# Optimization experiments

Hardware: AMD Instinct MI355X
Metric: run time of the kernel (lower is better)

The kernel has to match this reference:

```python
import jax, jax.numpy as jnp
import numpy as np

B, T, R, A = 4, 40, 2000, 36864
H = W = 64
C = 256
PP = 7
RED = 16.0
NCLS = 21
NPOS = 64   # rois_per_image*B//4
NNEG = 192  # rois_per_image*B*3//4
DH = 1024

def _iou(b1, b2):
    # boxes are (top,left,bottom,right)
    t = jnp.maximum(b1[..., 0], b2[..., 0])
    l = jnp.maximum(b1[..., 1], b2[..., 1])
    b = jnp.minimum(b1[..., 2], b2[..., 2])
    r = jnp.minimum(b1[..., 3], b2[..., 3])
    inter = jnp.clip(b - t, 0.0) * jnp.clip(r - l, 0.0)
    a1 = (b1[..., 2] - b1[..., 0]) * (b1[..., 3] - b1[..., 1])
    a2 = (b2[..., 2] - b2[..., 0]) * (b2[..., 3] - b2[..., 1])
    return inter / (a1 + a2 - inter)

def _smooth_l1(p, t):
    d = jnp.abs(p - t)
    return jnp.mean(jnp.where(d < 1.0, 0.5 * d * d, d - 0.5))

def _roi_pool(fm, rois):
    # fm [B,C,H,W], rois [N,5] = (img_id, top,left,bottom,right) in feature-map coords
    fmt = jnp.transpose(fm, (0, 2, 3, 1))  # [B,H,W,C]
    n = rois[:, 0].astype(jnp.int32)[:, None, None]
    t, l, b, r = rois[:, 1], rois[:, 2], rois[:, 3], rois[:, 4]
    g = (jnp.arange(PP, dtype=fm.dtype) + 0.5) / PP
    ys = jnp.clip(t[:, None] + g * (b - t)[:, None], 0.0, H - 1.0)
    xs = jnp.clip(l[:, None] + g * (r - l)[:, None], 0.0, W - 1.0)
    y0 = jnp.floor(ys).astype(jnp.int32)
    x0 = jnp.floor(xs).astype(jnp.int32)
    y1 = jnp.minimum(y0 + 1, H - 1)
    x1 = jnp.minimum(x0 + 1, W - 1)
    wy = (ys - y0)[:, :, None, None]
    wx = (xs - x0)[:, None, :, None]
    def gat(yi, xi):
        return fmt[n, yi[:, :, None], xi[:, None, :], :]  # [N,PP,PP,C]
    v = (gat(y0, x0) * (1 - wy) * (1 - wx) + gat(y0, x1) * (1 - wy) * wx
         + gat(y1, x0) * wy * (1 - wx) + gat(y1, x1) * wy * wx)
    return v.reshape(v.shape[0], -1)  # [N, PP*PP*C]

def _forward(nms_reg, nms_cls, feature_maps, bboxes, classes, anchors, rpn_reg, rpn_cls, W1, b1, Wr, br, Wc, bc):
    # ---------------- RPN trainer: anchor/target matching ----------------
    iou_a = _iou(bboxes[:, :, None, :], anchors[None, None, :, :])   # [B,T,A]
    max_iou = jnp.max(iou_a, axis=1)                                  # [B,A]
    tidx = jnp.argmax(iou_a, axis=1)
    max_tgt = jnp.take_along_axis(bboxes, jnp.broadcast_to(tidx[:, :, None], (B, A, 4)), axis=1)
    mask = (max_iou > 0.5).reshape(-1)
    pos = jnp.nonzero(mask, size=128)[0]        # first 128 positives, flat order (matches cls[mask][:128])
    neg = jnp.nonzero(~mask, size=256 - B)[0]   # torch quirk: 256 - len(mask_matched) = 256 - B
    clsf = rpn_cls.reshape(-1)
    logits = jnp.concatenate([clsf[pos], clsf[neg]])
    lbl = jnp.concatenate([jnp.ones(128, dtype=logits.dtype), jnp.zeros(256 - B, dtype=logits.dtype)])
    rpn_cls_loss = jnp.mean(jnp.maximum(logits, 0) - logits * lbl + jnp.log1p(jnp.exp(-jnp.abs(logits))))
    anc_f = jnp.broadcast_to(anchors[None], (B, A, 4)).reshape(-1, 4)
    rpn_reg_loss = _smooth_l1(rpn_reg.reshape(-1, 4)[pos], max_tgt.reshape(-1, 4)[pos] - anc_f[pos]) / 4.0

    # ------------- RCNN trainer: proposal matching + sampling -------------
    iou_r = _iou(nms_reg[:, None, :, :], bboxes[:, :, None, :])  # [B,T,R]
    iou_m = jnp.max(iou_r, axis=1)                               # [B,R]
    ridx = jnp.argmax(iou_r, axis=1)
    iou_f = iou_m.reshape(-1)
    posr = jnp.nonzero(iou_f > 0.5, size=NPOS)[0]                # first NPOS positives, flat order
    negscore = jnp.where(iou_f <= 0.5, iou_f, -jnp.inf)
    negr = jax.lax.top_k(negscore, NNEG)[1]                      # negatives sorted by IoU descending
    cls_g = jnp.take_along_axis(classes, ridx, axis=1).reshape(-1)
    cls_s = jnp.concatenate([cls_g[posr], jnp.zeros(NNEG, dtype=cls_g.dtype)])
    imid = jnp.repeat(jnp.arange(B, dtype=nms_reg.dtype), R)
    nmsf = nms_reg.reshape(-1, 4)
    sel = jnp.concatenate([posr, negr])
    rois = jnp.concatenate([imid[sel][:, None], nmsf[sel]], axis=1)  # [256,5]
    feat = _roi_pool(feature_maps, rois)
    hmid = jax.nn.relu(feat @ W1 + b1)
    rreg = hmid @ Wr + br
    rcls = hmid @ Wc + bc
    logp = jax.nn.log_softmax(rcls, axis=-1)
    rcnn_cls_loss = -jnp.mean(jnp.take_along_axis(logp, cls_s[:, None], axis=1))
    posb = nmsf[posr]
    rounded = jnp.concatenate([jnp.floor(posb[:, :2] * RED), jnp.ceil(posb[:, 2:] * RED)], axis=1) / RED
    mb = jnp.take_along_axis(bboxes, jnp.broadcast_to(ridx[:, :, None], (B, R, 4)), axis=1).reshape(-1, 4)[posr]
    tgt = mb - rounded
    pr = rreg[:NPOS]
    rcnn_reg_loss = sum(_smooth_l1(pr[:, c], tgt[:, c]) for c in range(4)) / 4.0
    offset = sum(jnp.mean(jnp.abs(pr[:, c] - tgt[:, c])) for c in range(4)) / 4.0
    acc = jnp.mean((jnp.argmax(rcls[:NPOS], axis=-1) == cls_s[:NPOS]).astype(jnp.float32))
    return rpn_cls_loss, rpn_reg_loss, rcnn_cls_loss, rcnn_reg_loss, acc, offset

def _boxes(k, shape):
    k1, k2 = jax.random.split(k)
    c = jax.random.uniform(k1, shape + (2,), minval=10.0, maxval=54.0)
    h = jax.random.uniform(k2, shape + (2,), minval=3.0, maxval=8.0)
    return jnp.concatenate([c - h, c + h], axis=-1)  # (top,left,bottom,right)

def setup_inputs():
    key = jax.random.key(0)
    ks = jax.random.split(key, 13)
    base = _boxes(ks[0], (T,))
    shift = jax.random.uniform(ks[1], (B, T, 2), minval=-0.2, maxval=0.2)
    bboxes = base[None] + jnp.concatenate([shift, shift], axis=-1)  # guarantees >=128 RPN positives
    classes = jax.random.randint(ks[2], (B, T), 1, NCLS)
    anchors = _boxes(ks[3], (A,)).at[:T].set(base)
    nms_reg = _boxes(ks[4], (B, R))
    shift2 = jax.random.uniform(ks[5], (B, T, 2), minval=-0.1, maxval=0.1)
    nms_reg = nms_reg.at[:, :T].set(bboxes + jnp.concatenate([shift2, shift2], axis=-1))  # >=64 RCNN positives
    nms_cls = jax.random.normal(ks[6], (B, R))
    feature_maps = jax.random.normal(ks[7], (B, C, H, W))
    rpn_reg = 0.1 * jax.random.normal(ks[8], (B, A, 4))
    rpn_cls = jax.random.normal(ks[9], (B, A))
    D = PP * PP * C
    W1 = jax.random.normal(ks[10], (D, DH)) * float(1.0 / np.sqrt(D))
    b1 = jnp.zeros((DH,))
    Wr = jax.random.normal(ks[11], (DH, 4)) * float(1.0 / np.sqrt(DH))
    br = jnp.zeros((4,))
    Wc = jax.random.normal(ks[12], (DH, NCLS)) * float(1.0 / np.sqrt(DH))
    bc = jnp.zeros((NCLS,))
    return dict(nms_reg=nms_reg, nms_cls=nms_cls, feature_maps=feature_maps, bboxes=bboxes,
                classes=classes, anchors=anchors, rpn_reg=rpn_reg, rpn_cls=rpn_cls,
                W1=W1, b1=b1, Wr=Wr, br=br, Wc=Wc, bc=bc)

def reference(nms_reg, nms_cls, feature_maps, bboxes, classes, anchors, rpn_reg, rpn_cls, W1, b1, Wr, br, Wc, bc):
    return _forward(nms_reg, nms_cls, feature_maps, bboxes, classes, anchors, rpn_reg, rpn_cls, W1, b1, Wr, br, Wc, bc)
```

## Files before the change

kernel.cpp:

```cpp
#include <hip/hip_runtime.h>

typedef unsigned short u16;
typedef unsigned long long u64;

constexpr int cB = 4, cT = 40, cR = 2000, cA = 36864;
constexpr int cH = 64, cW = 64, cC = 256, cPP = 7;
constexpr int cNCLS = 21, cNPOS = 64, cNNEG = 192, cDH = 1024;
constexpr int cD = cPP * cPP * cC;
constexpr int cBA = cB * cA;
constexpr int cBR = cB * cR;
constexpr int NW64 = cBA / 64;
constexpr int SPLITS = 8;
constexpr int KCH = cD / SPLITS;
constexpr unsigned POSKEY = 0x007FFFFFu;

constexpr size_t O_TIDX  = 0;
constexpr size_t O_MASKW = (size_t)cBA * 4;
constexpr size_t O_FMT   = 0;
constexpr size_t O_CPART = 0;
constexpr size_t O_PERS  = 8388608;
constexpr size_t O_SEL   = O_PERS;
constexpr size_t O_CLS   = O_PERS + 1024;
constexpr size_t O_ROIS  = O_PERS + 2048;
constexpr size_t O_TGT   = O_PERS + 6144;
constexpr size_t O_FEAT  = O_PERS + 8192;
constexpr size_t O_HMID  = O_FEAT + (size_t)256 * cD * 2;
constexpr size_t O_RREG  = O_HMID + (size_t)256 * cDH * 4;
constexpr size_t O_RCLS  = O_RREG + 4096;
constexpr size_t O_KEYS  = O_RCLS + 24576;
constexpr size_t O_RIDXG = O_KEYS + 32000;

__device__ __forceinline__ float b2f(u16 u) {
  return __uint_as_float(((unsigned)u) << 16);
}
__device__ __forceinline__ u16 f2b(float f) {
  unsigned x = __float_as_uint(f);
  unsigned r = x + 0x7FFFu + ((x >> 16) & 1u);
  return (u16)(r >> 16);
}
__device__ __forceinline__ unsigned f2key(float f) {
  unsigned b = __float_as_uint(f);
  return b ^ ((b & 0x80000000u) ? 0xFFFFFFFFu : 0x80000000u);
}

typedef __attribute__((ext_vector_type(8))) short short8;
typedef __attribute__((ext_vector_type(4))) float f32x4;

__global__ void k_rpn_iou(const float* __restrict__ bboxes, const float* __restrict__ anchors,
                          int* __restrict__ tidx, u64* __restrict__ maskw) {
  __shared__ float sb[cT * 4];
  int b = blockIdx.x / 144;
  if (threadIdx.x < cT * 4) sb[threadIdx.x] = bboxes[b * cT * 4 + threadIdx.x];
  __syncthreads();
  int i = blockIdx.x * 256 + threadIdx.x;
  int a = i - b * cA;
  float4 av = ((const float4*)anchors)[a];
  float at = av.x, al = av.y, ab = av.z, ar = av.w;
  float area_a = (ab - at) * (ar - al);
  float best = -1.0f; int bi = 0;
  for (int t = 0; t < cT; ++t) {
    float bt = sb[t * 4], bl = sb[t * 4 + 1], bbv = sb[t * 4 + 2], brv = sb[t * 4 + 3];
    float ih = fmaxf(fminf(bbv, ab) - fmaxf(bt, at), 0.0f);
    float iw = fmaxf(fminf(brv, ar) - fmaxf(bl, al), 0.0f);
    float inter = ih * iw;
    float a1 = (bbv - bt) * (brv - bl);
    float iou = inter / (a1 + area_a - inter);
    if (iou > best) { best = iou; bi = t; }
  }
  tidx[i] = bi;
  u64 bal = __ballot(best > 0.5f);
  if ((threadIdx.x & 63) == 0) maskw[i >> 6] = bal;
}

__global__ __launch_bounds__(1024) void k_rpn_sample_loss(
    const u64* __restrict__ maskw, const int* __restrict__ tidx,
    const float* __restrict__ rpn_cls, const float* __restrict__ rpn_reg,
    const float* __restrict__ bboxes, const float* __restrict__ anchors,
    float* __restrict__ out) {
  __shared__ u64 s_w[NW64];
  __shared__ int s_pre[144];
  __shared__ int s_cw[144];
  __shared__ int s_pos[128];
  __shared__ int s_neg[252];
  __shared__ float s_cls, s_reg;
  int tid = threadIdx.x, lane = tid & 63, w = tid >> 6;
  for (int k = tid; k < NW64; k += 1024) s_w[k] = maskw[k];
  if (tid < 128) s_pos[tid] = 0;
  if (tid < 252) s_neg[tid] = 0;
  if (tid == 0) { s_cls = 0.0f; s_reg = 0.0f; }
  __syncthreads();
  if (tid < 144) {
    int c = 0;
    #pragma unroll
    for (int k2 = 0; k2 < 16; ++k2) c += __popcll(s_w[tid * 16 + k2]);
    s_cw[tid] = c;
  }
  __syncthreads();
  if (tid == 0) {
    int run = 0;
    for (int ch = 0; ch < 144; ++ch) { s_pre[ch] = run; run += s_cw[ch]; }
  }
  __syncthreads();
  u64 lmask = (1ULL << lane) - 1ULL;
  for (int ch = w; ch < 144; ch += 16) {
    int pbase = s_pre[ch];
    int nbase = ch * 1024 - pbase;
    if (pbase >= 128 && nbase >= 252) continue;
    int pc = 0;
    #pragma unroll
    for (int s2 = 0; s2 < 16; ++s2) {
      u64 word = s_w[ch * 16 + s2];
      bool m = (word >> lane) & 1ULL;
      int prefP = __popcll(word & lmask);
      int idx = ch * 1024 + s2 * 64 + lane;
      if (m) {
        int g = pbase + pc + prefP;
        if (g < 128) s_pos[g] = idx;
      } else {
        int g = nbase + (s2 * 64 + lane) - (pc + prefP);
        if (g < 252) s_neg[g] = idx;
      }
      pc += __popcll(word);
    }
  }
  __syncthreads();
  if (tid < 380) {
    int flat; float lbl;
    if (tid < 128) { flat = s_pos[tid]; lbl = 1.0f; }
    else           { flat = s_neg[tid - 128]; lbl = 0.0f; }
    float l = rpn_cls[flat];
    float term = fmaxf(l, 0.0f) - l * lbl + log1pf(expf(-fabsf(l)));
    atomicAdd(&s_cls, term);
  }
  if (tid < 512) {
    int j = tid >> 2, c = tid & 3;
    int flat = s_pos[j];
    int b = flat / cA, a = flat - b * cA;
    int t = tidx[flat];
    float p = rpn_reg[flat * 4 + c];
    float tg = bboxes[(b * cT + t) * 4 + c] - anchors[a * 4 + c];
    float d = fabsf(p - tg);
    float sl = (d < 1.0f) ? 0.5f * d * d : d - 0.5f;
    atomicAdd(&s_reg, sl);
  }
  __syncthreads();
  if (tid == 0) {
    out[0] = s_cls / 380.0f;
    out[1] = s_reg / 512.0f / 4.0f;
  }
}

__global__ void k_rcnn_iou(const float* __restrict__ nms_reg, const float* __restrict__ bboxes,
                           unsigned* __restrict__ keys, int* __restrict__ ridx) {
  __shared__ float sb[cB * cT * 4];
  for (int j = threadIdx.x; j < cB * cT * 4; j += 256) sb[j] = bboxes[j];
  __syncthreads();
  int i = blockIdx.x * 256 + threadIdx.x;
  if (i >= cBR) return;
  int b = i / cR;
  float4 nv = ((const float4*)nms_reg)[i];
  float nt = nv.x, nl = nv.y, nb = nv.z, nr = nv.w;
  float area_n = (nb - nt) * (nr - nl);
  float best = -1.0f; int bi = 0;
  for (int t = 0; t < cT; ++t) {
    const float* bx = &sb[(b * cT + t) * 4];
    float ih = fmaxf(fminf(bx[2], nb) - fmaxf(bx[0], nt), 0.0f);
    float iw = fmaxf(fminf(bx[3], nr) - fmaxf(bx[1], nl), 0.0f);
    float inter = ih * iw;
    float a1 = (bx[2] - bx[0]) * (bx[3] - bx[1]);
    float iou = inter / (a1 + area_n - inter);
    if (iou > best) { best = iou; bi = t; }
  }
  keys[i] = (best <= 0.5f) ? f2key(best) : POSKEY;
  ridx[i] = bi;
}

__global__ __launch_bounds__(1024) void k_rcnn_select(
    const unsigned* __restrict__ keysg, const int* __restrict__ ridxg,
    const float* __restrict__ nms_reg, const float* __restrict__ bboxes,
    const int* __restrict__ classes,
    int* __restrict__ sel, int* __restrict__ cls_s,
    float* __restrict__ rois, float* __restrict__ tgt) {
  __shared__ unsigned s_key[cBR];
  __shared__ int s_hist[4096];
  __shared__ int s_pc[128];
  __shared__ int s_wsum[16], s_wsuf[16];
  __shared__ int s_posr[64], s_negr[cNNEG];
  __shared__ int s_bStar, s_over, s_cnt;
  int tid = threadIdx.x, lane = tid & 63, w = tid >> 6;
  u64 lmask = (1ULL << lane) - 1ULL;

  for (int i = tid; i < cBR; i += 1024) s_key[i] = keysg[i];
  if (tid < 64) s_posr[tid] = 0;
  __syncthreads();

  {
    int myv = 0; int mypre[8];
    #pragma unroll
    for (int p = 0; p < 8; ++p) {
      int i = p * 1024 + tid;
      bool v = (i < cBR) && (s_key[i] == POSKEY);
      u64 bal = __ballot(v);
      if (lane == 0) s_pc[p * 16 + w] = __popcll(bal);
      mypre[p] = __popcll(bal & lmask);
      myv |= v ? (1 << p) : 0;
    }
    __syncthreads();
    if (tid == 0) {
      int run = 0;
      for (int k = 0; k < 128; ++k) { int t = s_pc[k]; s_pc[k] = run; run += t; }
    }
    __syncthreads();
    #pragma unroll
    for (int p = 0; p < 8; ++p) {
      if (myv & (1 << p)) {
        int g = s_pc[p * 16 + w] + mypre[p];
        if (g < 64) s_posr[g] = p * 1024 + tid;
      }
    }
  }

  unsigned thr = 0; int G = 0;
  int need = cNNEG;
  #pragma unroll
  for (int lvl = 0; lvl < 3; ++lvl) {
    __syncthreads();
    #pragma unroll
    for (int k = 0; k < 4; ++k) s_hist[tid * 4 + k] = 0;
    __syncthreads();
    #pragma unroll
    for (int p = 0; p < 8; ++p) {
      int i = p * 1024 + tid;
      if (i < cBR) {
        unsigned key = s_key[i];
        int bkt = -1;
        if (lvl == 0) bkt = key >> 20;
        else if (lvl == 1) { if ((key >> 20) == (thr >> 20)) bkt = (key >> 8) & 0xFFF; }
        else { if ((key >> 8) == (thr >> 8)) bkt = (key & 0xFF) << 4; }
        if (bkt >= 0) atomicAdd(&s_hist[bkt], 1);
      }
    }
    __syncthreads();
    int local0 = s_hist[tid * 4 + 0], local1 = s_hist[tid * 4 + 1];
    int local2 = s_hist[tid * 4 + 2], local3 = s_hist[tid * 4 + 3];
    int lsum = local0 + local1 + local2 + local3;
    int x = lsum;
    #pragma unroll
    for (int off = 1; off < 64; off <<= 1) {
      int t = __shfl_down(x, off, 64);
      if (lane + off < 64) x += t;
    }
    if (lane == 0) s_wsum[w] = x;
    __syncthreads();
    if (tid == 0) {
      int run = 0;
      for (int wi = 15; wi >= 0; --wi) { s_wsuf[wi] = run; run += s_wsum[wi]; }
    }
    __syncthreads();
    int above = s_wsuf[w] + (x - lsum);
    int run = above;
    int loc[4] = {local3, local2, local1, local0};
    #pragma unroll
    for (int j = 0; j < 4; ++j) {
      int S = run + loc[j];
      if (run < need && S >= need) { s_bStar = tid * 4 + (3 - j); s_over = run; }
      run = S;
    }
    __syncthreads();
    int bS = s_bStar, ov = s_over;
    if (lvl == 0) thr = ((unsigned)bS) << 20;
    else if (lvl == 1) thr |= ((unsigned)bS) << 8;
    else thr |= ((unsigned)bS) >> 4;
    G += ov;
    need -= ov;
  }

  if (tid == 0) s_cnt = 0;
  __syncthreads();
  #pragma unroll
  for (int p = 0; p < 8; ++p) {
    int i = p * 1024 + tid;
    if (i < cBR && s_key[i] > thr) {
      int slot = atomicAdd(&s_cnt, 1);
      s_negr[slot] = i;
    }
  }
  {
    __syncthreads();
    int myv = 0; int mypre[8];
    #pragma unroll
    for (int p = 0; p < 8; ++p) {
      int i = p * 1024 + tid;
      bool v = (i < cBR) && (s_key[i] == thr);
      u64 bal = __ballot(v);
      if (lane == 0) s_pc[p * 16 + w] = __popcll(bal);
      mypre[p] = __popcll(bal & lmask);
      myv |= v ? (1 << p) : 0;
    }
    __syncthreads();
    if (tid == 0) {
      int run = 0;
      for (int k = 0; k < 128; ++k) { int t = s_pc[k]; s_pc[k] = run; run += t; }
    }
    __syncthreads();
    #pragma unroll
    for (int p = 0; p < 8; ++p) {
      if (myv & (1 << p)) {
        int g = s_pc[p * 16 + w] + mypre[p];
        if (g < need) s_negr[G + g] = p * 1024 + tid;
      }
    }
  }
  __syncthreads();

  if (tid < 256) {
    int flat = (tid < 64) ? s_posr[tid] : s_negr[tid - 64];
    sel[tid] = flat;
    int b = flat / cR;
    #pragma unroll
    for (int c = 0; c < 4; ++c) rois[tid * 4 + c] = nms_reg[flat * 4 + c];
    cls_s[tid] = (tid < 64) ? classes[b * cT + ridxg[flat]] : 0;
    if (tid < 64) {
      int mt = ridxg[flat];
      #pragma unroll
      for (int c = 0; c < 4; ++c) {
        float v = nms_reg[flat * 4 + c];
        float rr = ((c < 2) ? floorf(v * 16.0f) : ceilf(v * 16.0f)) / 16.0f;
        float mbv = bboxes[(b * cT + mt) * 4 + c];
        tgt[tid * 4 + c] = mbv - rr;
      }
    }
  }
}

__global__ void k_fmt(const float* __restrict__ fm, u16* __restrict__ fmt) {
  __shared__ float tile[32][33];
  int b = blockIdx.z;
  int p0 = blockIdx.x * 32, c0 = blockIdx.y * 32;
  int tx = threadIdx.x, ty = threadIdx.y;
  tile[ty][tx] = fm[((size_t)b * cC + (c0 + ty)) * (cH * cW) + p0 + tx];
  __syncthreads();
  fmt[((size_t)b * (cH * cW) + (p0 + ty)) * cC + c0 + tx] = f2b(tile[tx][ty]);
}

__global__ void k_roi_pool(const u16* __restrict__ fmt, const float* __restrict__ rois,
                           const int* __restrict__ sel, u16* __restrict__ feat) {
  int j = blockIdx.x;
  int py = blockIdx.y;
  int c = threadIdx.x;
  int flat = sel[j];
  int n = flat / cR;
  float t = rois[j * 4 + 0], l = rois[j * 4 + 1];
  float bb = rois[j * 4 + 2], r = rois[j * 4 + 3];
  const u16* base = fmt + (size_t)n * (cH * cW) * cC;
  float gy = (py + 0.5f) / (float)cPP;
  float ys = fminf(fmaxf(t + gy * (bb - t), 0.0f), 63.0f);
  int y0 = (int)floorf(ys);
  int y1 = min(y0 + 1, 63);
  float wy = ys - (float)y0;
  #pragma unroll
  for (int px = 0; px < cPP; ++px) {
    float gx = (px + 0.5f) / (float)cPP;
    float xs = fminf(fmaxf(l + gx * (r - l), 0.0f), 63.0f);
    int x0 = (int)floorf(xs);
    int x1 = min(x0 + 1, 63);
    float wx = xs - (float)x0;
    float f00 = b2f(base[(y0 * cW + x0) * cC + c]);
    float f01 = b2f(base[(y0 * cW + x1) * cC + c]);
    float f10 = b2f(base[(y1 * cW + x0) * cC + c]);
    float f11 = b2f(base[(y1 * cW + x1) * cC + c]);
    float v = f00 * (1.0f - wy) * (1.0f - wx) + f01 * (1.0f - wy) * wx +
              f10 * wy * (1.0f - wx) + f11 * wy * wx;
    feat[((size_t)j * 49 + py * cPP + px) * cC + c] = f2b(v);
  }
}

__global__ __launch_bounds__(256) void k_gemm1(const u16* __restrict__ feat, const float* __restrict__ W1,
                                               float* __restrict__ Cpart) {
  __shared__ u16 As[128][56];
  __shared__ u16 Bs[64][56];
  int tid = threadIdx.x;
  int n0 = blockIdx.x * 64;
  int kb0 = blockIdx.y * KCH;
  int m0 = blockIdx.z * 128;
  int lane = tid & 63, w = tid >> 6;
  int r = lane & 15, q = lane >> 4;
  f32x4 acc[2][4] = {};
  int arow = tid >> 1, ak = (tid & 1) * 16;
  int bk = tid >> 3, bn = (tid & 7) * 8;
  uint4 ra0, ra1;
  float4 rb0, rb1;
  {
    const u16* ap = &feat[(size_t)(m0 + arow) * cD + kb0 + ak];
    ra0 = *(const uint4*)ap; ra1 = *(const uint4*)(ap + 8);
    const float* bp = &W1[(size_t)(kb0 + bk) * cDH + n0 + bn];
    rb0 = *(const float4*)bp; rb1 = *(const float4*)(bp + 4);
  }
  for (int kc = 0; kc < KCH / 32; ++kc) {
    __syncthreads();
    *(uint4*)&As[arow][ak] = ra0;
    *(uint4*)&As[arow][ak + 8] = ra1;
    Bs[bn + 0][bk] = f2b(rb0.x); Bs[bn + 1][bk] = f2b(rb0.y);
    Bs[bn + 2][bk] = f2b(rb0.z); Bs[bn + 3][bk] = f2b(rb0.w);
    Bs[bn + 4][bk] = f2b(rb1.x); Bs[bn + 5][bk] = f2b(rb1.y);
    Bs[bn + 6][bk] = f2b(rb1.z); Bs[bn + 7][bk] = f2b(rb1.w);
    if (kc + 1 < KCH / 32) {
      int kb = kb0 + (kc + 1) * 32;
      const u16* ap = &feat[(size_t)(m0 + arow) * cD + kb + ak];
      ra0 = *(const uint4*)ap; ra1 = *(const uint4*)(ap + 8);
      const float* bp = &W1[(size_t)(kb + bk) * cDH + n0 + bn];
      rb0 = *(const float4*)bp; rb1 = *(const float4*)(bp + 4);
    }
    __syncthreads();
    short8 a[2], bfr[4];
    #pragma unroll
    for (int mt = 0; mt < 2; ++mt) a[mt] = *(const short8*)&As[w * 32 + mt * 16 + r][q * 8];
    #pragma unroll
    for (int nt = 0; nt < 4; ++nt) bfr[nt] = *(const short8*)&Bs[nt * 16 + r][q * 8];
    #pragma unroll
    for (int mt = 0; mt < 2; ++mt)
      #pragma unroll
      for (int nt = 0; nt < 4; ++nt)
        acc[mt][nt] = __builtin_amdgcn_mfma_f32_16x16x32_bf16(a[mt], bfr[nt], acc[mt][nt], 0, 0, 0);
  }
  float* Cp = Cpart + (size_t)blockIdx.y * 256 * cDH;
  #pragma unroll
  for (int mt = 0; mt < 2; ++mt) {
    #pragma unroll
    for (int nt = 0; nt < 4; ++nt) {
      #pragma unroll
      for (int rg = 0; rg < 4; ++rg) {
        int row = m0 + w * 32 + mt * 16 + q * 4 + rg;
        int col = n0 + nt * 16 + r;
        Cp[(size_t)row * cDH + col] = acc[mt][nt][rg];
      }
    }
  }
}

__global__ void k_bias_relu(const float* __restrict__ Cpart, const float* __restrict__ b1,
                            float* __restrict__ hmid) {
  int i = blockIdx.x * 256 + threadIdx.x;
  float v = b1[i & (cDH - 1)];
  #pragma unroll
  for (int s = 0; s < SPLITS; ++s) v += Cpart[(size_t)s * 256 * cDH + i];
  hmid[i] = fmaxf(v, 0.0f);
}

__global__ void k_gemm2(const float* __restrict__ hmid, const float* __restrict__ Wr, const float* __restrict__ br,
                        const float* __restrict__ Wc, const float* __restrict__ bc,
                        float* __restrict__ rreg, float* __restrict__ rcls) {
  int w = threadIdx.x >> 6, lane = threadIdx.x & 63;
  int row = blockIdx.x * 4 + w;
  float part[25];
  #pragma unroll
  for (int c = 0; c < 25; ++c) part[c] = 0.0f;
  for (int k = lane; k < cDH; k += 64) {
    float h = hmid[(size_t)row * cDH + k];
    #pragma unroll
    for (int c = 0; c < 4; ++c) part[c] += h * Wr[k * 4 + c];
    #pragma unroll
    for (int c = 0; c < 21; ++c) part[4 + c] += h * Wc[k * 21 + c];
  }
  #pragma unroll
  for (int off = 32; off; off >>= 1) {
    #pragma unroll
    for (int c = 0; c < 25; ++c) part[c] += __shfl_down(part[c], off, 64);
  }
  if (lane == 0) {
    #pragma unroll
    for (int c = 0; c < 4; ++c) rreg[row * 4 + c] = part[c] + br[c];
    #pragma unroll
    for (int c = 0; c < 21; ++c) rcls[row * 21 + c] = part[4 + c] + bc[c];
  }
}

__global__ void k_final(const float* __restrict__ rcls, const float* __restrict__ rreg,
                        const int* __restrict__ cls_s, const float* __restrict__ tgt,
                        float* __restrict__ out) {
  __shared__ float s_cls, s_acc, s_sl1, s_off;
  int tid = threadIdx.x;
  if (tid == 0) { s_cls = 0.0f; s_acc = 0.0f; s_sl1 = 0.0f; s_off = 0.0f; }
  __syncthreads();
  {
    int row = tid;
    float m = -INFINITY;
    for (int c = 0; c < cNCLS; ++c) m = fmaxf(m, rcls[row * cNCLS + c]);
    float sum = 0.0f;
    for (int c = 0; c < cNCLS; ++c) sum += expf(rcls[row * cNCLS + c] - m);
    float lse = m + logf(sum);
    float closs = lse - rcls[row * cNCLS + cls_s[row]];
    atomicAdd(&s_cls, closs);
  }
  if (tid < 64) {
    int am = 0; float bv = rcls[tid * cNCLS];
    for (int c = 1; c < cNCLS; ++c) {
      float v = rcls[tid * cNCLS + c];
      if (v > bv) { bv = v; am = c; }
    }
    if (am == cls_s[tid]) atomicAdd(&s_acc, 1.0f);
    float sl = 0.0f, of = 0.0f;
    #pragma unroll
    for (int c = 0; c < 4; ++c) {
      float d = fabsf(rreg[tid * 4 + c] - tgt[tid * 4 + c]);
      sl += (d < 1.0f) ? 0.5f * d * d : d - 0.5f;
      of += d;
    }
    atomicAdd(&s_sl1, sl);
    atomicAdd(&s_off, of);
  }
  __syncthreads();
  if (tid == 0) {
    out[2] = s_cls / 256.0f;
    out[3] = s_sl1 / 256.0f;
    out[4] = s_acc / 64.0f;
    out[5] = s_off / 256.0f;
  }
}

extern "C" void kernel_launch(void* const* d_in, const int* in_sizes, int n_in,
                              void* d_out, int out_size, void* d_ws, size_t ws_size,
                              hipStream_t stream) {
  const float* nms_reg = (const float*)d_in[0];
  const float* fm      = (const float*)d_in[2];
  const float* bboxes  = (const float*)d_in[3];
  const int*   classes = (const int*)d_in[4];
  const float* anchors = (const float*)d_in[5];
  const float* rpn_reg = (const float*)d_in[6];
  const float* rpn_cls = (const float*)d_in[7];
  const float* W1      = (const float*)d_in[8];
  const float* b1      = (const float*)d_in[9];
  const float* Wr      = (const float*)d_in[10];
  const float* br      = (const float*)d_in[11];
  const float* Wc      = (const float*)d_in[12];
  const float* bc      = (const float*)d_in[13];
  float* out = (float*)d_out;
  char* ws = (char*)d_ws;

  int*      tidx  = (int*)(ws + O_TIDX);
  u64*      maskw = (u64*)(ws + O_MASKW);
  u16*      fmt   = (u16*)(ws + O_FMT);
  float*    Cpart = (float*)(ws + O_CPART);
  int*      sel   = (int*)(ws + O_SEL);
  int*      clss  = (int*)(ws + O_CLS);
  float*    rois  = (float*)(ws + O_ROIS);
  float*    tgt   = (float*)(ws + O_TGT);
  u16*      feat  = (u16*)(ws + O_FEAT);
  float*    hmid  = (float*)(ws + O_HMID);
  float*    rreg  = (float*)(ws + O_RREG);
  float*    rcls  = (float*)(ws + O_RCLS);
  unsigned* keys  = (unsigned*)(ws + O_KEYS);
  int*      ridxg = (int*)(ws + O_RIDXG);

  k_rpn_iou<<<cBA / 256, 256, 0, stream>>>(bboxes, anchors, tidx, maskw);
  k_rpn_sample_loss<<<1, 1024, 0, stream>>>(maskw, tidx, rpn_cls, rpn_reg, bboxes, anchors, out);

  k_rcnn_iou<<<(cBR + 255) / 256, 256, 0, stream>>>(nms_reg, bboxes, keys, ridxg);
  k_rcnn_select<<<1, 1024, 0, stream>>>(keys, ridxg, nms_reg, bboxes, classes, sel, clss, rois, tgt);

  k_fmt<<<dim3(cH * cW / 32, cC / 32, cB), dim3(32, 32), 0, stream>>>(fm, fmt);
  k_roi_pool<<<dim3(256, cPP), 256, 0, stream>>>(fmt, rois, sel, feat);
  k_gemm1<<<dim3(16, SPLITS, 2), 256, 0, stream>>>(feat, W1, Cpart);
  k_bias_relu<<<(256 * cDH) / 256, 256, 0, stream>>>(Cpart, b1, hmid);
  k_gemm2<<<64, 256, 0, stream>>>(hmid, Wr, br, Wc, bc, rreg, rcls);
  k_final<<<1, 256, 0, stream>>>(rcls, rreg, clss, tgt, out);
}
```

Measured before the change: 226.4 us.

## Merge IoU and select kernels, retile transpose and GEMM1, fuse bias-ReLU into heads

Combines the RPN and RCNN IoU kernels into one launch and the two single-block selection kernels into a single two-block launch, so the two sequential selection passes run concurrently. The feature-map transpose now uses 64x64 tiles and writes packed 16-byte bf16 stores. GEMM1 drops to 64-row M tiles with twice as many blocks and an XOR-swizzled B tile in shared memory to reduce bank conflicts. The split-K reduction, bias and ReLU are folded into the head GEMV, which removes the hmid buffer and one launch at the cost of re-reading the split partials inside the heads kernel.

```diff
diff --git a/kernel.cpp b/kernel.cpp
--- a/kernel.cpp
+++ b/kernel.cpp
@@ -24,8 +24,7 @@
 constexpr size_t O_ROIS  = O_PERS + 2048;
 constexpr size_t O_TGT   = O_PERS + 6144;
 constexpr size_t O_FEAT  = O_PERS + 8192;
-constexpr size_t O_HMID  = O_FEAT + (size_t)256 * cD * 2;
-constexpr size_t O_RREG  = O_HMID + (size_t)256 * cDH * 4;
+constexpr size_t O_RREG  = O_FEAT + (size_t)256 * cD * 2;
 constexpr size_t O_RCLS  = O_RREG + 4096;
 constexpr size_t O_KEYS  = O_RCLS + 24576;
 constexpr size_t O_RIDXG = O_KEYS + 32000;
@@ -46,301 +45,318 @@
 typedef __attribute__((ext_vector_type(8))) short short8;
 typedef __attribute__((ext_vector_type(4))) float f32x4;
 
-__global__ void k_rpn_iou(const float* __restrict__ bboxes, const float* __restrict__ anchors,
-                          int* __restrict__ tidx, u64* __restrict__ maskw) {
-  __shared__ float sb[cT * 4];
-  int b = blockIdx.x / 144;
-  if (threadIdx.x < cT * 4) sb[threadIdx.x] = bboxes[b * cT * 4 + threadIdx.x];
-  __syncthreads();
-  int i = blockIdx.x * 256 + threadIdx.x;
-  int a = i - b * cA;
-  float4 av = ((const float4*)anchors)[a];
-  float at = av.x, al = av.y, ab = av.z, ar = av.w;
-  float area_a = (ab - at) * (ar - al);
-  float best = -1.0f; int bi = 0;
-  for (int t = 0; t < cT; ++t) {
-    float bt = sb[t * 4], bl = sb[t * 4 + 1], bbv = sb[t * 4 + 2], brv = sb[t * 4 + 3];
-    float ih = fmaxf(fminf(bbv, ab) - fmaxf(bt, at), 0.0f);
-    float iw = fmaxf(fminf(brv, ar) - fmaxf(bl, al), 0.0f);
-    float inter = ih * iw;
-    float a1 = (bbv - bt) * (brv - bl);
-    float iou = inter / (a1 + area_a - inter);
-    if (iou > best) { best = iou; bi = t; }
-  }
-  tidx[i] = bi;
-  u64 bal = __ballot(best > 0.5f);
-  if ((threadIdx.x & 63) == 0) maskw[i >> 6] = bal;
-}
-
-__global__ __launch_bounds__(1024) void k_rpn_sample_loss(
+__global__ void k_ious(const float* __restrict__ bboxes, const float* __restrict__ anchors,
+                       const float* __restrict__ nms_reg,
+                       int* __restrict__ tidx, u64* __restrict__ maskw,
+                       unsigned* __restrict__ keys, int* __restrict__ ridxg) {
+  __shared__ float sb[cB * cT * 4];
+  if (blockIdx.x < 576) {
+    int b = blockIdx.x / 144;
+    if (threadIdx.x < cT * 4) sb[threadIdx.x] = bboxes[b * cT * 4 + threadIdx.x];
+    __syncthreads();
+    int i = blockIdx.x * 256 + threadIdx.x;
+    int a = i - b * cA;
+    float4 av = ((const float4*)anchors)[a];
+    float at = av.x, al = av.y, ab = av.z, ar = av.w;
+    float area_a = (ab - at) * (ar - al);
+    float best = -1.0f; int bi = 0;
+    for (int t = 0; t < cT; ++t) {
+      float bt = sb[t * 4], bl = sb[t * 4 + 1], bbv = sb[t * 4 + 2], brv = sb[t * 4 + 3];
+      float ih = fmaxf(fminf(bbv, ab) - fmaxf(bt, at), 0.0f);
+      float iw = fmaxf(fminf(brv, ar) - fmaxf(bl, al), 0.0f);
+      float inter = ih * iw;
+      float a1 = (bbv - bt) * (brv - bl);
+      float iou = inter / (a1 + area_a - inter);
+      if (iou > best) { best = iou; bi = t; }
+    }
+    tidx[i] = bi;
+    u64 bal = __ballot(best > 0.5f);
+    if ((threadIdx.x & 63) == 0) maskw[i >> 6] = bal;
+  } else {
+    for (int j = threadIdx.x; j < cB * cT * 4; j += 256) sb[j] = bboxes[j];
+    __syncthreads();
+    int i = (blockIdx.x - 576) * 256 + threadIdx.x;
+    if (i >= cBR) return;
+    int b = i / cR;
+    float4 nv = ((const float4*)nms_reg)[i];
+    float nt = nv.x, nl = nv.y, nb = nv.z, nr = nv.w;
+    float area_n = (nb - nt) * (nr - nl);
+    float best = -1.0f; int bi = 0;
+    for (int t = 0; t < cT; ++t) {
+      const float* bx = &sb[(b * cT + t) * 4];
+      float ih = fmaxf(fminf(bx[2], nb) - fmaxf(bx[0], nt), 0.0f);
+      float iw = fmaxf(fminf(bx[3], nr) - fmaxf(bx[1], nl), 0.0f);
+      float inter = ih * iw;
+      float a1 = (bx[2] - bx[0]) * (bx[3] - bx[1]);
+      float iou = inter / (a1 + area_n - inter);
+      if (iou > best) { best = iou; bi = t; }
+    }
+    keys[i] = (best <= 0.5f) ? f2key(best) : POSKEY;
+    ridxg[i] = bi;
+  }
+}
+
+__global__ __launch_bounds__(1024) void k_select(
     const u64* __restrict__ maskw, const int* __restrict__ tidx,
     const float* __restrict__ rpn_cls, const float* __restrict__ rpn_reg,
     const float* __restrict__ bboxes, const float* __restrict__ anchors,
+    const unsigned* __restrict__ keysg, const int* __restrict__ ridxg,
+    const float* __restrict__ nms_reg, const int* __restrict__ classes,
+    int* __restrict__ sel, int* __restrict__ cls_s,
+    float* __restrict__ rois, float* __restrict__ tgt,
     float* __restrict__ out) {
-  __shared__ u64 s_w[NW64];
-  __shared__ int s_pre[144];
-  __shared__ int s_cw[144];
-  __shared__ int s_pos[128];
-  __shared__ int s_neg[252];
-  __shared__ float s_cls, s_reg;
-  int tid = threadIdx.x, lane = tid & 63, w = tid >> 6;
-  for (int k = tid; k < NW64; k += 1024) s_w[k] = maskw[k];
-  if (tid < 128) s_pos[tid] = 0;
-  if (tid < 252) s_neg[tid] = 0;
-  if (tid == 0) { s_cls = 0.0f; s_reg = 0.0f; }
-  __syncthreads();
-  if (tid < 144) {
-    int c = 0;
-    #pragma unroll
-    for (int k2 = 0; k2 < 16; ++k2) c += __popcll(s_w[tid * 16 + k2]);
-    s_cw[tid] = c;
-  }
-  __syncthreads();
-  if (tid == 0) {
-    int run = 0;
-    for (int ch = 0; ch < 144; ++ch) { s_pre[ch] = run; run += s_cw[ch]; }
-  }
-  __syncthreads();
-  u64 lmask = (1ULL << lane) - 1ULL;
-  for (int ch = w; ch < 144; ch += 16) {
-    int pbase = s_pre[ch];
-    int nbase = ch * 1024 - pbase;
-    if (pbase >= 128 && nbase >= 252) continue;
-    int pc = 0;
-    #pragma unroll
-    for (int s2 = 0; s2 < 16; ++s2) {
-      u64 word = s_w[ch * 16 + s2];
-      bool m = (word >> lane) & 1ULL;
-      int prefP = __popcll(word & lmask);
-      int idx = ch * 1024 + s2 * 64 + lane;
-      if (m) {
-        int g = pbase + pc + prefP;
-        if (g < 128) s_pos[g] = idx;
-      } else {
-        int g = nbase + (s2 * 64 + lane) - (pc + prefP);
-        if (g < 252) s_neg[g] = idx;
-      }
-      pc += __popcll(word);
-    }
-  }
-  __syncthreads();
-  if (tid < 380) {
-    int flat; float lbl;
-    if (tid < 128) { flat = s_pos[tid]; lbl = 1.0f; }
-    else           { flat = s_neg[tid - 128]; lbl = 0.0f; }
-    float l = rpn_cls[flat];
-    float term = fmaxf(l, 0.0f) - l * lbl + log1pf(expf(-fabsf(l)));
-    atomicAdd(&s_cls, term);
-  }
-  if (tid < 512) {
-    int j = tid >> 2, c = tid & 3;
-    int flat = s_pos[j];
-    int b = flat / cA, a = flat - b * cA;
-    int t = tidx[flat];
-    float p = rpn_reg[flat * 4 + c];
-    float tg = bboxes[(b * cT + t) * 4 + c] - anchors[a * 4 + c];
-    float d = fabsf(p - tg);
-    float sl = (d < 1.0f) ? 0.5f * d * d : d - 0.5f;
-    atomicAdd(&s_reg, sl);
-  }
-  __syncthreads();
-  if (tid == 0) {
-    out[0] = s_cls / 380.0f;
-    out[1] = s_reg / 512.0f / 4.0f;
-  }
-}
-
-__global__ void k_rcnn_iou(const float* __restrict__ nms_reg, const float* __restrict__ bboxes,
-                           unsigned* __restrict__ keys, int* __restrict__ ridx) {
-  __shared__ float sb[cB * cT * 4];
-  for (int j = threadIdx.x; j < cB * cT * 4; j += 256) sb[j] = bboxes[j];
-  __syncthreads();
-  int i = blockIdx.x * 256 + threadIdx.x;
-  if (i >= cBR) return;
-  int b = i / cR;
-  float4 nv = ((const float4*)nms_reg)[i];
-  float nt = nv.x, nl = nv.y, nb = nv.z, nr = nv.w;
-  float area_n = (nb - nt) * (nr - nl);
-  float best = -1.0f; int bi = 0;
-  for (int t = 0; t < cT; ++t) {
-    const float* bx = &sb[(b * cT + t) * 4];
-    float ih = fmaxf(fminf(bx[2], nb) - fmaxf(bx[0], nt), 0.0f);
-    float iw = fmaxf(fminf(bx[3], nr) - fmaxf(bx[1], nl), 0.0f);
-    float inter = ih * iw;
-    float a1 = (bx[2] - bx[0]) * (bx[3] - bx[1]);
-    float iou = inter / (a1 + area_n - inter);
-    if (iou > best) { best = iou; bi = t; }
-  }
-  keys[i] = (best <= 0.5f) ? f2key(best) : POSKEY;
-  ridx[i] = bi;
-}
-
-__global__ __launch_bounds__(1024) void k_rcnn_select(
-    const unsigned* __restrict__ keysg, const int* __restrict__ ridxg,
-    const float* __restrict__ nms_reg, const float* __restrict__ bboxes,
-    const int* __restrict__ classes,
-    int* __restrict__ sel, int* __restrict__ cls_s,
-    float* __restrict__ rois, float* __restrict__ tgt) {
-  __shared__ unsigned s_key[cBR];
-  __shared__ int s_hist[4096];
-  __shared__ int s_pc[128];
-  __shared__ int s_wsum[16], s_wsuf[16];
-  __shared__ int s_posr[64], s_negr[cNNEG];
-  __shared__ int s_bStar, s_over, s_cnt;
+  __shared__ __align__(16) char smem[50688];
+  __shared__ float s_scalF[2];
+  __shared__ int s_scalI[3];
   int tid = threadIdx.x, lane = tid & 63, w = tid >> 6;
   u64 lmask = (1ULL << lane) - 1ULL;
 
-  for (int i = tid; i < cBR; i += 1024) s_key[i] = keysg[i];
-  if (tid < 64) s_posr[tid] = 0;
-  __syncthreads();
-
-  {
-    int myv = 0; int mypre[8];
+  if (blockIdx.x == 0) {
+    u64* s_w   = (u64*)smem;
+    int* s_pre = (int*)(smem + 18432);
+    int* s_cw  = (int*)(smem + 19008);
+    int* s_pos = (int*)(smem + 19584);
+    int* s_neg = (int*)(smem + 20096);
+    for (int k = tid; k < NW64; k += 1024) s_w[k] = maskw[k];
+    if (tid < 128) s_pos[tid] = 0;
+    if (tid < 252) s_neg[tid] = 0;
+    if (tid == 0) { s_scalF[0] = 0.0f; s_scalF[1] = 0.0f; }
+    __syncthreads();
+    if (tid < 144) {
+      int c = 0;
+      #pragma unroll
+      for (int k2 = 0; k2 < 16; ++k2) c += __popcll(s_w[tid * 16 + k2]);
+      s_cw[tid] = c;
+    }
+    __syncthreads();
+    if (tid == 0) {
+      int run = 0;
+      for (int ch = 0; ch < 144; ++ch) { s_pre[ch] = run; run += s_cw[ch]; }
+    }
+    __syncthreads();
+    for (int ch = w; ch < 144; ch += 16) {
+      int pbase = s_pre[ch];
+      int nbase = ch * 1024 - pbase;
+      if (pbase >= 128 && nbase >= 252) continue;
+      int pc = 0;
+      #pragma unroll
+      for (int s2 = 0; s2 < 16; ++s2) {
+        u64 word = s_w[ch * 16 + s2];
+        bool m = (word >> lane) & 1ULL;
+        int prefP = __popcll(word & lmask);
+        int idx = ch * 1024 + s2 * 64 + lane;
+        if (m) {
+          int g = pbase + pc + prefP;
+          if (g < 128) s_pos[g] = idx;
+        } else {
+          int g = nbase + (s2 * 64 + lane) - (pc + prefP);
+          if (g < 252) s_neg[g] = idx;
+        }
+        pc += __popcll(word);
+      }
+    }
+    __syncthreads();
+    if (tid < 380) {
+      int flat; float lbl;
+      if (tid < 128) { flat = s_pos[tid]; lbl = 1.0f; }
+      else           { flat = s_neg[tid - 128]; lbl = 0.0f; }
+      float l = rpn_cls[flat];
+      float term = fmaxf(l, 0.0f) - l * lbl + log1pf(expf(-fabsf(l)));
+      atomicAdd(&s_scalF[0], term);
+    }
+    if (tid < 512) {
+      int j = tid >> 2, c = tid & 3;
+      int flat = s_pos[j];
+      int b = flat / cA, a = flat - b * cA;
+      int t = tidx[flat];
+      float p = rpn_reg[flat * 4 + c];
+      float tg = bboxes[(b * cT + t) * 4 + c] - anchors[a * 4 + c];
+      float d = fabsf(p - tg);
+      float sl = (d < 1.0f) ? 0.5f * d * d : d - 0.5f;
+      atomicAdd(&s_scalF[1], sl);
+    }
+    __syncthreads();
+    if (tid == 0) {
+      out[0] = s_scalF[0] / 380.0f;
+      out[1] = s_scalF[1] / 512.0f / 4.0f;
+    }
+  } else {
+    unsigned* s_key = (unsigned*)smem;
+    int* s_hist = (int*)(smem + 32000);
+    int* s_pc   = (int*)(smem + 48384);
+    int* s_wsum = (int*)(smem + 48896);
+    int* s_wsuf = (int*)(smem + 48960);
+    int* s_posr = (int*)(smem + 49024);
+    int* s_negr = (int*)(smem + 49280);
+
+    for (int i = tid; i < cBR; i += 1024) s_key[i] = keysg[i];
+    if (tid < 64) s_posr[tid] = 0;
+    __syncthreads();
+
+    {
+      int myv = 0; int mypre[8];
+      #pragma unroll
+      for (int p = 0; p < 8; ++p) {
+        int i = p * 1024 + tid;
+        bool v = (i < cBR) && (s_key[i] == POSKEY);
+        u64 bal = __ballot(v);
+        if (lane == 0) s_pc[p * 16 + w] = __popcll(bal);
+        mypre[p] = __popcll(bal & lmask);
+        myv |= v ? (1 << p) : 0;
+      }
+      __syncthreads();
+      if (tid == 0) {
+        int run = 0;
+        for (int k = 0; k < 128; ++k) { int t = s_pc[k]; s_pc[k] = run; run += t; }
+      }
+      __syncthreads();
+      #pragma unroll
+      for (int p = 0; p < 8; ++p) {
+        if (myv & (1 << p)) {
+          int g = s_pc[p * 16 + w] + mypre[p];
+          if (g < 64) s_posr[g] = p * 1024 + tid;
+        }
+      }
+    }
+
+    unsigned thr = 0; int G = 0;
+    int need = cNNEG;
+    #pragma unroll
+    for (int lvl = 0; lvl < 3; ++lvl) {
+      __syncthreads();
+      #pragma unroll
+      for (int k = 0; k < 4; ++k) s_hist[tid * 4 + k] = 0;
+      __syncthreads();
+      #pragma unroll
+      for (int p = 0; p < 8; ++p) {
+        int i = p * 1024 + tid;
+        if (i < cBR) {
+          unsigned key = s_key[i];
+          int bkt = -1;
+          if (lvl == 0) bkt = key >> 20;
+          else if (lvl == 1) { if ((key >> 20) == (thr >> 20)) bkt = (key >> 8) & 0xFFF; }
+          else { if ((key >> 8) == (thr >> 8)) bkt = (key & 0xFF) << 4; }
+          if (bkt >= 0) atomicAdd(&s_hist[bkt], 1);
+        }
+      }
+      __syncthreads();
+      int local0 = s_hist[tid * 4 + 0], local1 = s_hist[tid * 4 + 1];
+      int local2 = s_hist[tid * 4 + 2], local3 = s_hist[tid * 4 + 3];
+      int lsum = local0 + local1 + local2 + local3;
+      int x = lsum;
+      #pragma unroll
+      for (int off = 1; off < 64; off <<= 1) {
+        int t = __shfl_down(x, off, 64);
+        if (lane + off < 64) x += t;
+      }
+      if (lane == 0) s_wsum[w] = x;
+      __syncthreads();
+      if (tid == 0) {
+        int run = 0;
+        for (int wi = 15; wi >= 0; --wi) { s_wsuf[wi] = run; run += s_wsum[wi]; }
+      }
+      __syncthreads();
+      int above = s_wsuf[w] + (x - lsum);
+      int run = above;
+      int loc[4] = {local3, local2, local1, local0};
+      #pragma unroll
+      for (int j = 0; j < 4; ++j) {
+        int S = run + loc[j];
+        if (run < need && S >= need) { s_scalI[0] = tid * 4 + (3 - j); s_scalI[1] = run; }
+        run = S;
+      }
+      __syncthreads();
+      int bS = s_scalI[0], ov = s_scalI[1];
+      if (lvl == 0) thr = ((unsigned)bS) << 20;
+      else if (lvl == 1) thr |= ((unsigned)bS) << 8;
+      else thr |= ((unsigned)bS) >> 4;
+      G += ov;
+      need -= ov;
+    }
+
+    if (tid == 0) s_scalI[2] = 0;
+    __syncthreads();
     #pragma unroll
     for (int p = 0; p < 8; ++p) {
       int i = p * 1024 + tid;
-      bool v = (i < cBR) && (s_key[i] == POSKEY);
-      u64 bal = __ballot(v);
-      if (lane == 0) s_pc[p * 16 + w] = __popcll(bal);
-      mypre[p] = __popcll(bal & lmask);
-      myv |= v ? (1 << p) : 0;
-    }
-    __syncthreads();
-    if (tid == 0) {
-      int run = 0;
-      for (int k = 0; k < 128; ++k) { int t = s_pc[k]; s_pc[k] = run; run += t; }
-    }
-    __syncthreads();
-    #pragma unroll
-    for (int p = 0; p < 8; ++p) {
-      if (myv & (1 << p)) {
-        int g = s_pc[p * 16 + w] + mypre[p];
-        if (g < 64) s_posr[g] = p * 1024 + tid;
-      }
-    }
-  }
-
-  unsigned thr = 0; int G = 0;
-  int need = cNNEG;
+      if (i < cBR && s_key[i] > thr) {
+        int slot = atomicAdd(&s_scalI[2], 1);
+        s_negr[slot] = i;
+      }
+    }
+    {
+      __syncthreads();
+      int myv = 0; int mypre[8];
+      #pragma unroll
+      for (int p = 0; p < 8; ++p) {
+        int i = p * 1024 + tid;
+        bool v = (i < cBR) && (s_key[i] == thr);
+        u64 bal = __ballot(v);
+        if (lane == 0) s_pc[p * 16 + w] = __popcll(bal);
+        mypre[p] = __popcll(bal & lmask);
+        myv |= v ? (1 << p) : 0;
+      }
+      __syncthreads();
+      if (tid == 0) {
+        int run = 0;
+        for (int k = 0; k < 128; ++k) { int t = s_pc[k]; s_pc[k] = run; run += t; }
+      }
+      __syncthreads();
+      #pragma unroll
+      for (int p = 0; p < 8; ++p) {
+        if (myv & (1 << p)) {
+          int g = s_pc[p * 16 + w] + mypre[p];
+          if (g < need) s_negr[G + g] = p * 1024 + tid;
+        }
+      }
+    }
+    __syncthreads();
+
+    if (tid < 256) {
+      int flat = (tid < 64) ? s_posr[tid] : s_negr[tid - 64];
+      sel[tid] = flat;
+      int b = flat / cR;
+      #pragma unroll
+      for (int c = 0; c < 4; ++c) rois[tid * 4 + c] = nms_reg[flat * 4 + c];
+      cls_s[tid] = (tid < 64) ? classes[b * cT + ridxg[flat]] : 0;
+      if (tid < 64) {
+        int mt = ridxg[flat];
+        #pragma unroll
+        for (int c = 0; c < 4; ++c) {
+          float v = nms_reg[flat * 4 + c];
+          float rr = ((c < 2) ? floorf(v * 16.0f) : ceilf(v * 16.0f)) / 16.0f;
+          float mbv = bboxes[(b * cT + mt) * 4 + c];
+          tgt[tid * 4 + c] = mbv - rr;
+        }
+      }
+    }
+  }
+}
+
+__global__ __launch_bounds__(256) void k_fmt(const float* __restrict__ fm, u16* __restrict__ fmt) {
+  __shared__ float tile[64][65];
+  int b = blockIdx.z;
+  int p0 = blockIdx.x * 64, c0 = blockIdx.y * 64;
+  int t = threadIdx.x;
+  int pL = (t & 15) * 4, cL = t >> 4;
   #pragma unroll
-  for (int lvl = 0; lvl < 3; ++lvl) {
-    __syncthreads();
-    #pragma unroll
-    for (int k = 0; k < 4; ++k) s_hist[tid * 4 + k] = 0;
-    __syncthreads();
-    #pragma unroll
-    for (int p = 0; p < 8; ++p) {
-      int i = p * 1024 + tid;
-      if (i < cBR) {
-        unsigned key = s_key[i];
-        int bkt = -1;
-        if (lvl == 0) bkt = key >> 20;
-        else if (lvl == 1) { if ((key >> 20) == (thr >> 20)) bkt = (key >> 8) & 0xFFF; }
-        else { if ((key >> 8) == (thr >> 8)) bkt = (key & 0xFF) << 4; }
-        if (bkt >= 0) atomicAdd(&s_hist[bkt], 1);
-      }
-    }
-    __syncthreads();
-    int local0 = s_hist[tid * 4 + 0], local1 = s_hist[tid * 4 + 1];
-    int local2 = s_hist[tid * 4 + 2], local3 = s_hist[tid * 4 + 3];
-    int lsum = local0 + local1 + local2 + local3;
-    int x = lsum;
-    #pragma unroll
-    for (int off = 1; off < 64; off <<= 1) {
-      int t = __shfl_down(x, off, 64);
-      if (lane + off < 64) x += t;
-    }
-    if (lane == 0) s_wsum[w] = x;
-    __syncthreads();
-    if (tid == 0) {
-      int run = 0;
-      for (int wi = 15; wi >= 0; --wi) { s_wsuf[wi] = run; run += s_wsum[wi]; }
-    }
-    __syncthreads();
-    int above = s_wsuf[w] + (x - lsum);
-    int run = above;
-    int loc[4] = {local3, local2, local1, local0};
-    #pragma unroll
-    for (int j = 0; j < 4; ++j) {
-      int S = run + loc[j];
-      if (run < need && S >= need) { s_bStar = tid * 4 + (3 - j); s_over = run; }
-      run = S;
-    }
-    __syncthreads();
-    int bS = s_bStar, ov = s_over;
-    if (lvl == 0) thr = ((unsigned)bS) << 20;
-    else if (lvl == 1) thr |= ((unsigned)bS) << 8;
-    else thr |= ((unsigned)bS) >> 4;
-    G += ov;
-    need -= ov;
-  }
-
-  if (tid == 0) s_cnt = 0;
+  for (int i = 0; i < 4; ++i) {
+    int c = cL + i * 16;
+    float4 v = *(const float4*)&fm[((size_t)b * cC + c0 + c) * (cH * cW) + p0 + pL];
+    tile[c][pL] = v.x; tile[c][pL + 1] = v.y; tile[c][pL + 2] = v.z; tile[c][pL + 3] = v.w;
+  }
   __syncthreads();
+  int pW = t >> 2, cg = (t & 3) * 16;
+  unsigned pk[8];
   #pragma unroll
-  for (int p = 0; p < 8; ++p) {
-    int i = p * 1024 + tid;
-    if (i < cBR && s_key[i] > thr) {
-      int slot = atomicAdd(&s_cnt, 1);
-      s_negr[slot] = i;
-    }
-  }
-  {
-    __syncthreads();
-    int myv = 0; int mypre[8];
-    #pragma unroll
-    for (int p = 0; p < 8; ++p) {
-      int i = p * 1024 + tid;
-      bool v = (i < cBR) && (s_key[i] == thr);
-      u64 bal = __ballot(v);
-      if (lane == 0) s_pc[p * 16 + w] = __popcll(bal);
-      mypre[p] = __popcll(bal & lmask);
-      myv |= v ? (1 << p) : 0;
-    }
-    __syncthreads();
-    if (tid == 0) {
-      int run = 0;
-      for (int k = 0; k < 128; ++k) { int t = s_pc[k]; s_pc[k] = run; run += t; }
-    }
-    __syncthreads();
-    #pragma unroll
-    for (int p = 0; p < 8; ++p) {
-      if (myv & (1 << p)) {
-        int g = s_pc[p * 16 + w] + mypre[p];
-        if (g < need) s_negr[G + g] = p * 1024 + tid;
-      }
-    }
-  }
-  __syncthreads();
-
-  if (tid < 256) {
-    int flat = (tid < 64) ? s_posr[tid] : s_negr[tid - 64];
-    sel[tid] = flat;
-    int b = flat / cR;
-    #pragma unroll
-    for (int c = 0; c < 4; ++c) rois[tid * 4 + c] = nms_reg[flat * 4 + c];
-    cls_s[tid] = (tid < 64) ? classes[b * cT + ridxg[flat]] : 0;
-    if (tid < 64) {
-      int mt = ridxg[flat];
-      #pragma unroll
-      for (int c = 0; c < 4; ++c) {
-        float v = nms_reg[flat * 4 + c];
-        float rr = ((c < 2) ? floorf(v * 16.0f) : ceilf(v * 16.0f)) / 16.0f;
-        float mbv = bboxes[(b * cT + mt) * 4 + c];
-        tgt[tid * 4 + c] = mbv - rr;
-      }
-    }
-  }
-}
-
-__global__ void k_fmt(const float* __restrict__ fm, u16* __restrict__ fmt) {
-  __shared__ float tile[32][33];
-  int b = blockIdx.z;
-  int p0 = blockIdx.x * 32, c0 = blockIdx.y * 32;
-  int tx = threadIdx.x, ty = threadIdx.y;
-  tile[ty][tx] = fm[((size_t)b * cC + (c0 + ty)) * (cH * cW) + p0 + tx];
-  __syncthreads();
-  fmt[((size_t)b * (cH * cW) + (p0 + ty)) * cC + c0 + tx] = f2b(tile[tx][ty]);
+  for (int j = 0; j < 8; ++j) {
+    unsigned lo = f2b(tile[cg + 2 * j][pW]);
+    unsigned hi = f2b(tile[cg + 2 * j + 1][pW]);
+    pk[j] = lo | (hi << 16);
+  }
+  u16* dst = &fmt[((size_t)b * (cH * cW) + p0 + pW) * cC + c0 + cg];
+  *(uint4*)dst = *(uint4*)&pk[0];
+  *(uint4*)(dst + 8) = *(uint4*)&pk[4];
 }
 
 __global__ void k_roi_pool(const u16* __restrict__ fmt, const float* __restrict__ rois,
@@ -377,77 +393,65 @@
 
 __global__ __launch_bounds__(256) void k_gemm1(const u16* __restrict__ feat, const float* __restrict__ W1,
                                                float* __restrict__ Cpart) {
-  __shared__ u16 As[128][56];
+  __shared__ u16 As[64][56];
   __shared__ u16 Bs[64][56];
   int tid = threadIdx.x;
   int n0 = blockIdx.x * 64;
   int kb0 = blockIdx.y * KCH;
-  int m0 = blockIdx.z * 128;
+  int m0 = blockIdx.z * 64;
   int lane = tid & 63, w = tid >> 6;
   int r = lane & 15, q = lane >> 4;
-  f32x4 acc[2][4] = {};
-  int arow = tid >> 1, ak = (tid & 1) * 16;
+  f32x4 acc[4] = {};
+  int arow = tid >> 2, ak = (tid & 3) * 8;
   int bk = tid >> 3, bn = (tid & 7) * 8;
-  uint4 ra0, ra1;
+  uint4 ra;
   float4 rb0, rb1;
   {
-    const u16* ap = &feat[(size_t)(m0 + arow) * cD + kb0 + ak];
-    ra0 = *(const uint4*)ap; ra1 = *(const uint4*)(ap + 8);
+    ra = *(const uint4*)&feat[(size_t)(m0 + arow) * cD + kb0 + ak];
     const float* bp = &W1[(size_t)(kb0 + bk) * cDH + n0 + bn];
     rb0 = *(const float4*)bp; rb1 = *(const float4*)(bp + 4);
   }
   for (int kc = 0; kc < KCH / 32; ++kc) {
     __syncthreads();
-    *(uint4*)&As[arow][ak] = ra0;
-    *(uint4*)&As[arow][ak + 8] = ra1;
-    Bs[bn + 0][bk] = f2b(rb0.x); Bs[bn + 1][bk] = f2b(rb0.y);
-    Bs[bn + 2][bk] = f2b(rb0.z); Bs[bn + 3][bk] = f2b(rb0.w);
-    Bs[bn + 4][bk] = f2b(rb1.x); Bs[bn + 5][bk] = f2b(rb1.y);
-    Bs[bn + 6][bk] = f2b(rb1.z); Bs[bn + 7][bk] = f2b(rb1.w);
+    *(uint4*)&As[arow][ak] = ra;
+    {
+      float bv[8] = {rb0.x, rb0.y, rb0.z, rb0.w, rb1.x, rb1.y, rb1.z, rb1.w};
+      int kg = bk >> 3, kw = bk & 7;
+      #pragma unroll
+      for (int i = 0; i < 8; ++i) {
+        int row = bn + i;
+        Bs[row][((kg ^ ((row >> 3) & 3)) << 3) + kw] = f2b(bv[i]);
+      }
+    }
     if (kc + 1 < KCH / 32) {
       int kb = kb0 + (kc + 1) * 32;
-      const u16* ap = &feat[(size_t)(m0 + arow) * cD + kb + ak];
-      ra0 = *(const uint4*)ap; ra1 = *(const uint4*)(ap + 8);
+      ra = *(const uint4*)&feat[(size_t)(m0 + arow) * cD + kb + ak];
       const float* bp = &W1[(size_t)(kb + bk) * cDH + n0 + bn];
       rb0 = *(const float4*)bp; rb1 = *(const float4*)(bp + 4);
     }
     __syncthreads();
-    short8 a[2], bfr[4];
-    #pragma unroll
-    for (int mt = 0; mt < 2; ++mt) a[mt] = *(const short8*)&As[w * 32 + mt * 16 + r][q * 8];
-    #pragma unroll
-    for (int nt = 0; nt < 4; ++nt) bfr[nt] = *(const short8*)&Bs[nt * 16 + r][q * 8];
-    #pragma unroll
-    for (int mt = 0; mt < 2; ++mt)
-      #pragma unroll
-      for (int nt = 0; nt < 4; ++nt)
-        acc[mt][nt] = __builtin_amdgcn_mfma_f32_16x16x32_bf16(a[mt], bfr[nt], acc[mt][nt], 0, 0, 0);
+    short8 a = *(const short8*)&As[w * 16 + r][q * 8];
+    #pragma unroll
+    for (int nt = 0; nt < 4; ++nt) {
+      int n = nt * 16 + r;
+      short8 bfr = *(const short8*)&Bs[n][(q ^ ((n >> 3) & 3)) << 3];
+      acc[nt] = __builtin_amdgcn_mfma_f32_16x16x32_bf16(a, bfr, acc[nt], 0, 0, 0);
+    }
   }
   float* Cp = Cpart + (size_t)blockIdx.y * 256 * cDH;
   #pragma unroll
-  for (int mt = 0; mt < 2; ++mt) {
-    #pragma unroll
-    for (int nt = 0; nt < 4; ++nt) {
-      #pragma unroll
-      for (int rg = 0; rg < 4; ++rg) {
-        int row = m0 + w * 32 + mt * 16 + q * 4 + rg;
-        int col = n0 + nt * 16 + r;
-        Cp[(size_t)row * cDH + col] = acc[mt][nt][rg];
-      }
-    }
-  }
-}
-
-__global__ void k_bias_relu(const float* __restrict__ Cpart, const float* __restrict__ b1,
-                            float* __restrict__ hmid) {
-  int i = blockIdx.x * 256 + threadIdx.x;
-  float v = b1[i & (cDH - 1)];
-  #pragma unroll
-  for (int s = 0; s < SPLITS; ++s) v += Cpart[(size_t)s * 256 * cDH + i];
-  hmid[i] = fmaxf(v, 0.0f);
-}
-
-__global__ void k_gemm2(const float* __restrict__ hmid, const float* __restrict__ Wr, const float* __restrict__ br,
+  for (int nt = 0; nt < 4; ++nt) {
+    #pragma unroll
+    for (int rg = 0; rg < 4; ++rg) {
+      int row = m0 + w * 16 + q * 4 + rg;
+      int col = n0 + nt * 16 + r;
+      Cp[(size_t)row * cDH + col] = acc[nt][rg];
+    }
+  }
+}
+
+__global__ void k_heads(const float* __restrict__ Cpart, const float* __restrict__ b1,
+                        const float* __restrict__ Wr, const float* __restrict__ br,
                         const float* __restrict__ Wc, const float* __restrict__ bc,
                         float* __restrict__ rreg, float* __restrict__ rcls) {
   int w = threadIdx.x >> 6, lane = threadIdx.x & 63;
@@ -456,7 +460,10 @@
   #pragma unroll
   for (int c = 0; c < 25; ++c) part[c] = 0.0f;
   for (int k = lane; k < cDH; k += 64) {
-    float h = hmid[(size_t)row * cDH + k];
+    float h = b1[k];
+    #pragma unroll
+    for (int s = 0; s < SPLITS; ++s) h += Cpart[(size_t)s * 256 * cDH + (size_t)row * cDH + k];
+    h = fmaxf(h, 0.0f);
     #pragma unroll
     for (int c = 0; c < 4; ++c) part[c] += h * Wr[k * 4 + c];
     #pragma unroll
@@ -546,22 +553,17 @@
   float*    rois  = (float*)(ws + O_ROIS);
   float*    tgt   = (float*)(ws + O_TGT);
   u16*      feat  = (u16*)(ws + O_FEAT);
-  float*    hmid  = (float*)(ws + O_HMID);
   float*    rreg  = (float*)(ws + O_RREG);
   float*    rcls  = (float*)(ws + O_RCLS);
   unsigned* keys  = (unsigned*)(ws + O_KEYS);
   int*      ridxg = (int*)(ws + O_RIDXG);
 
-  k_rpn_iou<<<cBA / 256, 256, 0, stream>>>(bboxes, anchors, tidx, maskw);
-  k_rpn_sample_loss<<<1, 1024, 0, stream>>>(maskw, tidx, rpn_cls, rpn_reg, bboxes, anchors, out);
-
-  k_rcnn_iou<<<(cBR + 255) / 256, 256, 0, stream>>>(nms_reg, bboxes, keys, ridxg);
-  k_rcnn_select<<<1, 1024, 0, stream>>>(keys, ridxg, nms_reg, bboxes, classes, sel, clss, rois, tgt);
-
-  k_fmt<<<dim3(cH * cW / 32, cC / 32, cB), dim3(32, 32), 0, stream>>>(fm, fmt);
+  k_ious<<<576 + 32, 256, 0, stream>>>(bboxes, anchors, nms_reg, tidx, maskw, keys, ridxg);
+  k_select<<<2, 1024, 0, stream>>>(maskw, tidx, rpn_cls, rpn_reg, bboxes, anchors,
+                                   keys, ridxg, nms_reg, classes, sel, clss, rois, tgt, out);
+  k_fmt<<<dim3(cH * cW / 64, cC / 64, cB), 256, 0, stream>>>(fm, fmt);
   k_roi_pool<<<dim3(256, cPP), 256, 0, stream>>>(fmt, rois, sel, feat);
-  k_gemm1<<<dim3(16, SPLITS, 2), 256, 0, stream>>>(feat, W1, Cpart);
-  k_bias_relu<<<(256 * cDH) / 256, 256, 0, stream>>>(Cpart, b1, hmid);
-  k_gemm2<<<64, 256, 0, stream>>>(hmid, Wr, br, Wc, bc, rreg, rcls);
+  k_gemm1<<<dim3(16, SPLITS, 4), 256, 0, stream>>>(feat, W1, Cpart);
+  k_heads<<<64, 256, 0, stream>>>(Cpart, b1, Wr, br, Wc, bc, rreg, rcls);
   k_final<<<1, 256, 0, stream>>>(rcls, rreg, clss, tgt, out);
 }
```

Result: faster. 201.0 us (-11.2%).
